# Kernel tuning notes

Hardware: AMD Instinct MI355X
Metric: run time of the kernel (lower is better)

Reference implementation:

```python
import jax, jax.numpy as jnp
import numpy as np

NAF, NBF, DT = 64, 32, 1
B, GROUP = 2000, 100
P = B * GROUP

def _lin(key, din, dout):
    kw, kb = jax.random.split(key)
    return (jax.random.normal(kw, (din, dout), jnp.float32) * 0.02,
            jax.random.normal(kb, (dout,), jnp.float32) * 0.01)

def setup_inputs() -> dict:
    key = jax.random.key(0)
    ks = jax.random.split(key, 12)
    pairs = jax.random.normal(ks[0], (P, 2 * NAF + NBF), jnp.float32)
    idx_pairs = jnp.full((B,), GROUP, dtype=jnp.int32)
    ref_feats = jax.random.normal(ks[1], (B, 32), jnp.float32)
    aw, ab = _lin(ks[2], NAF, 128)
    bw, bb = _lin(ks[3], NBF, 128)
    p1w, p1b = _lin(ks[4], 384, 512)
    p2w, p2b = _lin(ks[5], 512, 256)
    p3w, p3b = _lin(ks[6], 256, 1024)
    f1w, f1b = _lin(ks[7], 1024, 512)
    f2w, f2b = _lin(ks[8], 512, 32)
    f3w, f3b = _lin(ks[9], 32, DT)
    return dict(pairs=pairs, idx_pairs=idx_pairs, ref_feats=ref_feats,
                aw=aw, ab=ab, bw=bw, bb=bb,
                p1w=p1w, p1b=p1b, p2w=p2w, p2b=p2b, p3w=p3w, p3b=p3b,
                f1w=f1w, f1b=f1b, f2w=f2w, f2b=f2b, f3w=f3w, f3b=f3b)

def reference(pairs, idx_pairs, ref_feats,
              aw, ab, bw, bb,
              p1w, p1b, p2w, p2b, p3w, p3b,
              f1w, f1b, f2w, f2b, f3w, f3b):
    relu = jax.nn.relu
    a1 = relu(pairs[:, :NAF] @ aw + ab)            # [P,128]
    a2 = relu(pairs[:, NAF:2 * NAF] @ aw + ab)     # [P,128]
    be = relu(pairs[:, 2 * NAF:] @ bw + bb)        # [P,128]
    h = jnp.concatenate([a1, a2, be], axis=1)      # [P,384]
    h = relu(h @ p1w + p1b)
    h = relu(h @ p2w + p2b)
    x = h @ p3w + p3b                              # [P,1024]
    nb = idx_pairs.shape[0]
    seg = jnp.repeat(jnp.arange(nb, dtype=jnp.int32), idx_pairs,
                     total_repeat_length=x.shape[0])
    sums = jax.ops.segment_sum(x, seg, num_segments=nb)
    h_pair = sums / idx_pairs[:, None].astype(x.dtype)  # segment mean [B,1024]
    h = relu(h_pair @ f1w + f1b)
    h = relu(h @ f2w + f2b)
    return h @ f3w + f3b                           # [B,1]
```

## Files before the change

### kernel.cpp

```cpp
#include <hip/hip_runtime.h>
#include <cstdint>
#include <cstddef>


typedef __bf16 bf16;
typedef __attribute__((ext_vector_type(8))) __bf16 bf16x8;
typedef __attribute__((ext_vector_type(4))) __bf16 bf16x4;
typedef __attribute__((ext_vector_type(4))) float floatx4;
typedef __attribute__((ext_vector_type(16))) float floatx16;

#define GRP 100
#define NWIN 3125

#define WOFF_AW 0
#define WOFF_BW 8192
#define WOFF_P1 12288
#define WOFF_P2 208896
#define WOFF_P3 339968
#define WOFF_F1 602112
#define WOFF_F2 1126400
#define WOFF_HS 1142784

#define LSTR_P  168
#define LSTR_H  392
#define LSTR_H2 136
#define LSTR_MS 264

static __device__ __forceinline__ floatx4 mfma16(bf16x8 a, bf16x8 b, floatx4 c) {
  return __builtin_amdgcn_mfma_f32_16x16x32_bf16(a, b, c, 0, 0, 0);
}
static __device__ __forceinline__ floatx16 mfma32(bf16x8 a, bf16x8 b, floatx16 c) {
  return __builtin_amdgcn_mfma_f32_32x32x16_bf16(a, b, c, 0, 0, 0);
}

static __device__ __forceinline__ void gload(floatx4& d, const bf16* p) {
  asm volatile("global_load_dwordx4 %0, %1, off" : "=v"(d) : "v"(p));
}
static __device__ __forceinline__ bf16x8 bc8(floatx4 v) {
  return __builtin_bit_cast(bf16x8, v);
}

#define VMW(N)                                         \
  do {                                                 \
    asm volatile("s_waitcnt vmcnt(" #N ")");           \
    __builtin_amdgcn_sched_barrier(0);                 \
  } while (0)

#define SYNCL()                                        \
  do {                                                 \
    asm volatile("s_waitcnt lgkmcnt(0)" ::: "memory"); \
    __builtin_amdgcn_s_barrier();                      \
  } while (0)

__global__ __launch_bounds__(256) void pack_lds(
    const float* __restrict__ aw, const float* __restrict__ bw,
    const float* __restrict__ p1w, const float* __restrict__ p2w,
    const float* __restrict__ p3w, const float* __restrict__ f1w,
    const float* __restrict__ f2w, bf16* __restrict__ wpk) {
  __shared__ float t[32][65];
  const int tid = threadIdx.x;
  int b = blockIdx.x;

  if (b < 550) {
    const float* src; int dstoff, K, N, tt;
    bool newf = false;
    if (b < 4)        { src = aw;  dstoff = WOFF_AW; K = 64;   N = 128;  tt = b; }
    else if (b < 6)   { src = bw;  dstoff = WOFF_BW; K = 32;   N = 128;  tt = b - 4; }
    else if (b < 102) { src = p1w; dstoff = WOFF_P1; K = 384;  N = 512;  tt = b - 6;   newf = true; }
    else if (b < 166) { src = p2w; dstoff = WOFF_P2; K = 512;  N = 256;  tt = b - 102; newf = true; }
    else if (b < 294) { src = p3w; dstoff = WOFF_P3; K = 256;  N = 1024; tt = b - 166; }
    else              { src = f1w; dstoff = WOFF_F1; K = 1024; N = 512;  tt = b - 294; }
    const int KT = K >> 5;
    const int kt = tt % KT;
    const int n0 = (tt / KT) * 64;
    for (int i = tid; i < 2048; i += 256) {
      int r = i >> 6, c = i & 63;
      t[r][c] = src[(size_t)(kt * 32 + r) * N + n0 + c];
    }
    __syncthreads();
    if (newf) {
      const int cpp = tid & 63, rb = tid >> 6;
      const int g = (n0 >> 5) + (cpp >> 5);
      const int c = cpp & 31;
      bf16x8 v;
#pragma unroll
      for (int i = 0; i < 8; ++i) v[i] = (bf16)t[rb * 8 + i][cpp];
      *(bf16x8*)(wpk + dstoff +
                 (((size_t)g * KT + kt) * 2 + (rb >> 1)) * 512 +
                 (c + 32 * (rb & 1)) * 8) = v;
    } else {
      const int nc = n0 >> 7, nl0 = n0 & 127;
      bf16* dst = wpk + dstoff + ((size_t)(nc * KT + kt) * 128 + nl0) * 32;
      int o = tid * 8;
      int nl = o >> 5, kk = o & 31;
      bf16x8 v;
#pragma unroll
      for (int i = 0; i < 8; ++i) v[i] = (bf16)t[kk + i][nl];
      *(bf16x8*)(dst + nl * 32 + kk) = v;
    }
  } else {
    const int kt = b - 550;
    for (int i = tid; i < 1024; i += 256) {
      int r = i >> 5, c = i & 31;
      t[r][c] = f2w[(size_t)(kt * 32 + r) * 32 + c];
    }
    __syncthreads();
    if (tid < 128) {
      int o = tid * 8;
      int nl = o >> 5, kk = o & 31;
      bf16x8 v;
#pragma unroll
      for (int i = 0; i < 8; ++i) v[i] = (bf16)t[kk + i][nl];
      *(bf16x8*)(wpk + WOFF_F2 + kt * 1024 + nl * 32 + kk) = v;
    }
  }
}

static __device__ __forceinline__ void kstep2(const bf16* __restrict__ Ab,
                                              int astride, int acol,
                                              const bf16* __restrict__ b0p,
                                              const bf16* __restrict__ b1p,
                                              floatx4* acc, int lm, int lq) {
  bf16x8 b0 = *(const bf16x8*)b0p;
  bf16x8 b1 = *(const bf16x8*)b1p;
#pragma unroll
  for (int mt = 0; mt < 4; ++mt) {
    bf16x8 a = *(const bf16x8*)(Ab + (mt * 16 + lm) * astride + acol + lq * 8);
    acc[mt * 2]     = mfma16(a, b0, acc[mt * 2]);
    acc[mt * 2 + 1] = mfma16(a, b1, acc[mt * 2 + 1]);
  }
}

static __device__ __forceinline__ void epi2(const floatx4* acc,
                                            const float* __restrict__ bias,
                                            bf16* dst, int dstride, int w,
                                            int lm, int lq) {
#pragma unroll
  for (int mt = 0; mt < 4; ++mt)
#pragma unroll
    for (int j = 0; j < 2; ++j) {
      int col = (w + 4 * j) * 16 + lm;
      float bv = bias[col];
      floatx4 c = acc[mt * 2 + j];
#pragma unroll
      for (int r = 0; r < 4; ++r) {
        float v = c[r] + bv;
        v = v > 0.f ? v : 0.f;
        dst[(mt * 16 + lq * 4 + r) * dstride + col] = (bf16)v;
      }
    }
}

__global__ __launch_bounds__(256, 2) void seg_kernel(
    const float* __restrict__ pairs, const float* __restrict__ ab,
    const float* __restrict__ bb, const float* __restrict__ p1b,
    const float* __restrict__ p2b, const bf16* __restrict__ wpk,
    float* __restrict__ hsum) {
  __shared__ __align__(16) bf16 hbuf[64 * LSTR_H];
  __shared__ __align__(16) bf16 pbuf[64 * LSTR_P];

  const int tid = threadIdx.x;
  const int w = tid >> 6;
  const int lane = tid & 63;
  const int lm = lane & 15;
  const int lq = lane >> 4;
  const int l31 = lane & 31;
  const int hi = lane >> 5;
  const int hi8 = hi * 8;
  const int ln8 = lane * 8;
  const int blk = blockIdx.x;

  {
    const float4* src = (const float4*)(pairs + (size_t)blk * (64 * 160));
    for (int i = tid; i < 64 * 40; i += 256) {
      int row = i / 40;
      int c4 = (i - row * 40) * 4;
      float4 v = src[i];
      bf16x4 o = {(bf16)v.x, (bf16)v.y, (bf16)v.z, (bf16)v.w};
      *(bf16x4*)(pbuf + row * LSTR_P + c4) = o;
    }
  }
  SYNCL();

  const floatx4 fz = {0.f, 0.f, 0.f, 0.f};
  const floatx16 fz16 = {0.f, 0.f, 0.f, 0.f, 0.f, 0.f, 0.f, 0.f,
                         0.f, 0.f, 0.f, 0.f, 0.f, 0.f, 0.f, 0.f};
  floatx4 acc[8];

#pragma unroll
  for (int t = 0; t < 8; ++t) acc[t] = fz;
#pragma unroll
  for (int kt = 0; kt < 2; ++kt)
    kstep2(pbuf, LSTR_P, kt * 32,
           wpk + WOFF_AW + ((size_t)(kt * 128 + w * 16 + lm)) * 32 + lq * 8,
           wpk + WOFF_AW + ((size_t)(kt * 128 + (w + 4) * 16 + lm)) * 32 + lq * 8,
           acc, lm, lq);
  epi2(acc, ab, hbuf, LSTR_H, w, lm, lq);
#pragma unroll
  for (int t = 0; t < 8; ++t) acc[t] = fz;
#pragma unroll
  for (int kt = 0; kt < 2; ++kt)
    kstep2(pbuf, LSTR_P, 64 + kt * 32,
           wpk + WOFF_AW + ((size_t)(kt * 128 + w * 16 + lm)) * 32 + lq * 8,
           wpk + WOFF_AW + ((size_t)(kt * 128 + (w + 4) * 16 + lm)) * 32 + lq * 8,
           acc, lm, lq);
  epi2(acc, ab, hbuf + 128, LSTR_H, w, lm, lq);
#pragma unroll
  for (int t = 0; t < 8; ++t) acc[t] = fz;
  kstep2(pbuf, LSTR_P, 128,
         wpk + WOFF_BW + ((size_t)(w * 16 + lm)) * 32 + lq * 8,
         wpk + WOFF_BW + ((size_t)((w + 4) * 16 + lm)) * 32 + lq * 8,
         acc, lm, lq);
  epi2(acc, bb, hbuf + 256, LSTR_H, w, lm, lq);

  float p1bv[4], p2bv[2];
#pragma unroll
  for (int nc = 0; nc < 4; ++nc) p1bv[nc] = p1b[nc * 128 + w * 32 + l31];
  p2bv[0] = p2b[w * 32 + l31];
  p2bv[1] = p2b[(w + 4) * 32 + l31];
  asm volatile("" : "+v"(p1bv[0]), "+v"(p1bv[1]), "+v"(p1bv[2]),
                    "+v"(p1bv[3]), "+v"(p2bv[0]), "+v"(p2bv[1]));

  floatx4 p1r0[4], p1r1[4];
  floatx4 p2r[3][4];
  floatx16 acc3[4];

#pragma unroll
  for (int q = 0; q < 3; ++q) {
    gload(p1r0[q], wpk + WOFF_P1 + (((size_t)w * 12 + q) * 2 + 0) * 512 + ln8);
    gload(p1r1[q], wpk + WOFF_P1 + (((size_t)w * 12 + q) * 2 + 1) * 512 + ln8);
  }
  SYNCL();

#pragma unroll
  for (int t = 0; t < 4; ++t) acc3[t] = fz16;

#pragma unroll
  for (int nc = 0; nc < 4; ++nc) {
    const int gw = nc * 4 + w;
    floatx16 acc2[2];
    acc2[0] = fz16; acc2[1] = fz16;

    {
      bf16x8 an[2][4];
#pragma unroll
      for (int q = 0; q < 2; ++q)
#pragma unroll
        for (int rg = 0; rg < 2; ++rg)
#pragma unroll
          for (int h = 0; h < 2; ++h)
            an[q][rg * 2 + h] = *(const bf16x8*)(
                hbuf + (rg * 32 + l31) * LSTR_H + q * 32 + h * 16 + hi8);
#pragma unroll
      for (int kt = 0; kt < 12; ++kt) {
        bf16x8 a00 = an[kt & 1][0], a01 = an[kt & 1][1];
        bf16x8 a10 = an[kt & 1][2], a11 = an[kt & 1][3];
        if (kt < 10) {
#pragma unroll
          for (int rg = 0; rg < 2; ++rg)
#pragma unroll
            for (int h = 0; h < 2; ++h)
              an[kt & 1][rg * 2 + h] = *(const bf16x8*)(
                  hbuf + (rg * 32 + l31) * LSTR_H + (kt + 2) * 32 + h * 16 + hi8);
        }
        if (kt < 9) {
          gload(p1r0[(kt + 3) & 3],
                wpk + WOFF_P1 + (((size_t)gw * 12 + kt + 3) * 2 + 0) * 512 + ln8);
          gload(p1r1[(kt + 3) & 3],
                wpk + WOFF_P1 + (((size_t)gw * 12 + kt + 3) * 2 + 1) * 512 + ln8);
        }
        if (kt < 9)       { VMW(6); }
        else if (kt == 9) { VMW(4); }
        else if (kt == 10){ VMW(2); }
        else              { VMW(0); }
        __builtin_amdgcn_s_setprio(1);
        bf16x8 b0 = bc8(p1r0[kt & 3]);
        bf16x8 b1 = bc8(p1r1[kt & 3]);
        acc2[0] = mfma32(a00, b0, acc2[0]);
        acc2[1] = mfma32(a10, b0, acc2[1]);
        acc2[0] = mfma32(a01, b1, acc2[0]);
        acc2[1] = mfma32(a11, b1, acc2[1]);
        __builtin_amdgcn_s_setprio(0);
      }
    }

#pragma unroll
    for (int q = 0; q < 2; ++q)
#pragma unroll
      for (int cg = 0; cg < 2; ++cg)
#pragma unroll
        for (int h = 0; h < 2; ++h)
          gload(p2r[q][cg * 2 + h],
                wpk + WOFF_P2 +
                    (((size_t)(cg ? w + 4 : w) * 16 + nc * 4 + q) * 2 + h) * 512 +
                    ln8);

    SYNCL();
    {
      float bv = p1bv[nc];
#pragma unroll
      for (int rg = 0; rg < 2; ++rg)
#pragma unroll
        for (int r = 0; r < 16; ++r) {
          float v = acc2[rg][r] + bv;
          v = v > 0.f ? v : 0.f;
          int row = rg * 32 + (r & 3) + 8 * (r >> 2) + 4 * hi;
          pbuf[row * LSTR_H2 + w * 32 + l31] = (bf16)v;
        }
    }
    SYNCL();

    {
      bf16x8 an2[2][4];
#pragma unroll
      for (int q = 0; q < 2; ++q)
#pragma unroll
        for (int rg = 0; rg < 2; ++rg)
#pragma unroll
          for (int h = 0; h < 2; ++h)
            an2[q][rg * 2 + h] = *(const bf16x8*)(
                pbuf + (rg * 32 + l31) * LSTR_H2 + q * 32 + h * 16 + hi8);
#pragma unroll
      for (int kt2 = 0; kt2 < 4; ++kt2) {
        bf16x8 ac[4];
#pragma unroll
        for (int f = 0; f < 4; ++f) ac[f] = an2[kt2 & 1][f];
        if (kt2 < 2) {
#pragma unroll
          for (int rg = 0; rg < 2; ++rg)
#pragma unroll
            for (int h = 0; h < 2; ++h)
              an2[kt2 & 1][rg * 2 + h] = *(const bf16x8*)(
                  pbuf + (rg * 32 + l31) * LSTR_H2 + (kt2 + 2) * 32 + h * 16 + hi8);
#pragma unroll
          for (int cg = 0; cg < 2; ++cg)
#pragma unroll
            for (int h = 0; h < 2; ++h)
              gload(p2r[(kt2 + 2) % 3][cg * 2 + h],
                    wpk + WOFF_P2 +
                        (((size_t)(cg ? w + 4 : w) * 16 + nc * 4 + kt2 + 2) * 2 + h) *
                            512 + ln8);
        }
        if (kt2 == 1) {
          const int gn = ((nc + 1) & 3) * 4 + w;
#pragma unroll
          for (int q = 0; q < 3; ++q) {
            gload(p1r0[q],
                  wpk + WOFF_P1 + (((size_t)gn * 12 + q) * 2 + 0) * 512 + ln8);
            gload(p1r1[q],
                  wpk + WOFF_P1 + (((size_t)gn * 12 + q) * 2 + 1) * 512 + ln8);
          }
        }
        if (kt2 == 0)      { VMW(8); }
        else if (kt2 == 1) { VMW(14); }
        else if (kt2 == 2) { VMW(10); }
        else               { VMW(6); }
        __builtin_amdgcn_s_setprio(1);
#pragma unroll
        for (int h = 0; h < 2; ++h) {
          bf16x8 b0 = bc8(p2r[kt2 % 3][0 * 2 + h]);
          bf16x8 b1 = bc8(p2r[kt2 % 3][1 * 2 + h]);
          acc3[0] = mfma32(ac[0 * 2 + h], b0, acc3[0]);
          acc3[1] = mfma32(ac[0 * 2 + h], b1, acc3[1]);
          acc3[2] = mfma32(ac[1 * 2 + h], b0, acc3[2]);
          acc3[3] = mfma32(ac[1 * 2 + h], b1, acc3[3]);
        }
        __builtin_amdgcn_s_setprio(0);
      }
    }
  }

  const int s0 = (64 * blk) / 100;
  const int sp = (s0 + 1) * 100 - 64 * blk;

#pragma unroll
  for (int cg = 0; cg < 2; ++cg) {
    float bv = p2bv[cg];
    float tot = 0.f, cs0 = 0.f;
#pragma unroll
    for (int rg = 0; rg < 2; ++rg)
#pragma unroll
      for (int r = 0; r < 16; ++r) {
        float v = acc3[rg * 2 + cg][r] + bv;
        v = v > 0.f ? v : 0.f;
        tot += v;
        int row = rg * 32 + (r & 3) + 8 * (r >> 2) + 4 * hi;
        cs0 += (row < sp) ? v : 0.f;
      }
    float cs1 = tot - cs0;
    cs0 += __shfl_xor(cs0, 32, 64);
    cs1 += __shfl_xor(cs1, 32, 64);
    if (lane < 32) {
      int col = (cg ? w + 4 : w) * 32 + lane;
      hsum[(size_t)(2 * blk) * 256 + col]     = cs0;
      hsum[(size_t)(2 * blk + 1) * 256 + col] = cs1;
    }
  }
}

__global__ __launch_bounds__(512, 2) void tail_kernel(
    const bf16* __restrict__ wpk, const float* __restrict__ hsum,
    const int* __restrict__ idxp, const float* __restrict__ p3b,
    const float* __restrict__ f1b, const float* __restrict__ f2b,
    const float* __restrict__ f3w, const float* __restrict__ f3b,
    float* __restrict__ out) {
  __shared__ __align__(16) bf16 ms[16 * LSTR_MS];
  __shared__ __align__(16) bf16 hp[16 * 1032];
  __shared__ __align__(16) bf16 h2s[16 * 520];
  __shared__ __align__(16) bf16 h3s[16 * 40];

  const int tid = threadIdx.x;
  const int w = tid >> 6;
  const int lane = tid & 63;
  const int lm = lane & 15;
  const int lq = lane >> 4;
  const int r0 = blockIdx.x * 16;
  const floatx4 fz = {0.f, 0.f, 0.f, 0.f};

  for (int i = tid; i < 16 * 64; i += 512) {
    int row = i >> 6, c4 = i & 63;
    int seg = r0 + row;
    int b_lo = (100 * seg) >> 6;
    int b_hi = (100 * seg + 99) >> 6;
    float4 sa = {0.f, 0.f, 0.f, 0.f};
    for (int b = b_lo; b <= b_hi; ++b) {
      int slot = (64 * b >= 100 * seg) ? 0 : 1;
      float4 v = *(const float4*)(hsum + (size_t)(2 * b + slot) * 256 + c4 * 4);
      sa.x += v.x; sa.y += v.y; sa.z += v.z; sa.w += v.w;
    }
    float inv = 1.f / (float)idxp[seg];
    bf16x4 o = {(bf16)(sa.x * inv), (bf16)(sa.y * inv),
                (bf16)(sa.z * inv), (bf16)(sa.w * inv)};
    *(bf16x4*)(ms + row * LSTR_MS + c4 * 4) = o;
  }
  __syncthreads();

#pragma unroll
  for (int nt2 = 0; nt2 < 4; ++nt2) {
    floatx4 a2[2];
    a2[0] = fz; a2[1] = fz;
#pragma unroll
    for (int kt = 0; kt < 8; ++kt) {
      bf16x8 a = *(const bf16x8*)(ms + lm * LSTR_MS + kt * 32 + lq * 8);
#pragma unroll
      for (int j = 0; j < 2; ++j) {
        bf16x8 b = *(const bf16x8*)(wpk + WOFF_P3 +
            ((size_t)((w * 8 + kt) * 128 + (nt2 * 2 + j) * 16 + lm)) * 32 +
            lq * 8);
        a2[j] = mfma16(a, b, a2[j]);
      }
    }
#pragma unroll
    for (int j = 0; j < 2; ++j) {
      int col = w * 128 + (nt2 * 2 + j) * 16 + lm;
      float bv = p3b[col];
#pragma unroll
      for (int r = 0; r < 4; ++r)
        hp[(lq * 4 + r) * 1032 + col] = (bf16)(a2[j][r] + bv);
    }
  }
  __syncthreads();

  {
    floatx4 a4[4];
#pragma unroll
    for (int j = 0; j < 4; ++j) a4[j] = fz;
#pragma unroll 8
    for (int kt = 0; kt < 32; ++kt) {
      bf16x8 a = *(const bf16x8*)(hp + lm * 1032 + kt * 32 + lq * 8);
#pragma unroll
      for (int j = 0; j < 4; ++j) {
        bf16x8 b = *(const bf16x8*)(wpk + WOFF_F1 +
            ((size_t)(((w >> 1) * 32 + kt) * 128 + (w & 1) * 64 + j * 16 + lm)) * 32 +
            lq * 8);
        a4[j] = mfma16(a, b, a4[j]);
      }
    }
#pragma unroll
    for (int j = 0; j < 4; ++j) {
      int col = w * 64 + j * 16 + lm;
      float bv = f1b[col];
#pragma unroll
      for (int r = 0; r < 4; ++r) {
        float v = a4[j][r] + bv;
        v = v > 0.f ? v : 0.f;
        h2s[(lq * 4 + r) * 520 + col] = (bf16)v;
      }
    }
  }
  __syncthreads();

  if (w < 2) {
    floatx4 c2 = fz;
#pragma unroll
    for (int kt = 0; kt < 16; ++kt) {
      bf16x8 a = *(const bf16x8*)(h2s + lm * 520 + kt * 32 + lq * 8);
      bf16x8 b = *(const bf16x8*)(wpk + WOFF_F2 +
                    ((size_t)(kt * 32 + w * 16 + lm)) * 32 + lq * 8);
      c2 = mfma16(a, b, c2);
    }
    int col = w * 16 + lm;
    float bv = f2b[col];
#pragma unroll
    for (int r = 0; r < 4; ++r) {
      float v = c2[r] + bv;
      v = v > 0.f ? v : 0.f;
      h3s[(lq * 4 + r) * 40 + col] = (bf16)v;
    }
  }
  __syncthreads();
  if (w == 0) {
    float ps = 0.f;
#pragma unroll
    for (int jj = 0; jj < 8; ++jj)
      ps += (float)h3s[lm * 40 + lq * 8 + jj] * f3w[lq * 8 + jj];
    ps += __shfl_xor(ps, 16, 64);
    ps += __shfl_xor(ps, 32, 64);
    if (lq == 0) out[r0 + lm] = ps + f3b[0];
  }
}

extern "C" void kernel_launch(void* const* d_in, const int* in_sizes, int n_in,
                              void* d_out, int out_size, void* d_ws,
                              size_t ws_size, hipStream_t stream) {
  (void)in_sizes; (void)n_in; (void)out_size; (void)ws_size;
  const float* pairs = (const float*)d_in[0];
  const int*   idxp  = (const int*)d_in[1];
  const float* aw  = (const float*)d_in[3];
  const float* ab  = (const float*)d_in[4];
  const float* bw  = (const float*)d_in[5];
  const float* bb  = (const float*)d_in[6];
  const float* p1w = (const float*)d_in[7];
  const float* p1b = (const float*)d_in[8];
  const float* p2w = (const float*)d_in[9];
  const float* p2b = (const float*)d_in[10];
  const float* p3w = (const float*)d_in[11];
  const float* p3b = (const float*)d_in[12];
  const float* f1w = (const float*)d_in[13];
  const float* f1b = (const float*)d_in[14];
  const float* f2w = (const float*)d_in[15];
  const float* f2b = (const float*)d_in[16];
  const float* f3w = (const float*)d_in[17];
  const float* f3b = (const float*)d_in[18];

  bf16* wpk = (bf16*)d_ws;
  float* hsum = (float*)(wpk + WOFF_HS);

  pack_lds<<<566, 256, 0, stream>>>(aw, bw, p1w, p2w, p3w, f1w, f2w, wpk);
  seg_kernel<<<NWIN, 256, 0, stream>>>(pairs, ab, bb, p1b, p2b, wpk, hsum);
  tail_kernel<<<125, 512, 0, stream>>>(wpk, hsum, idxp, p3b, f1b, f2b, f3w,
                                       f3b, (float*)d_out);
}
```

Measured before the change: 386.0 us.

## Swizzle LDS layouts, double-buffer p1 output, and move embed layers to 32x32 MFMA

Replaces padded LDS strides with an XOR-swizzled unpadded layout for the input, hidden and intermediate buffers. The intermediate p1 output now alternates between two LDS halves, which removes one block barrier per chunk. The embedding layers are rewritten to use 32x32 MFMA with prepacked weights loaded through the global-load pipeline, so they share the p1 layer's packing format. The aim is fewer bank conflicts, fewer barriers and better latency hiding, at the cost of more complex addressing and higher register use.

Result: slower. 682.2 us (+76.7%).

```diff
diff --git a/kernel.cpp b/kernel.cpp
--- a/kernel.cpp
+++ b/kernel.cpp
@@ -21,10 +21,9 @@
 #define WOFF_F2 1126400
 #define WOFF_HS 1142784
 
-#define LSTR_P  168
-#define LSTR_H  392
-#define LSTR_H2 136
 #define LSTR_MS 264
+
+#define SWZ(row, off) ((off) ^ (((row) & 7) << 4))
 
 static __device__ __forceinline__ floatx4 mfma16(bf16x8 a, bf16x8 b, floatx4 c) {
   return __builtin_amdgcn_mfma_f32_16x16x32_bf16(a, b, c, 0, 0, 0);
@@ -38,6 +37,9 @@
 }
 static __device__ __forceinline__ bf16x8 bc8(floatx4 v) {
   return __builtin_bit_cast(bf16x8, v);
+}
+static __device__ __forceinline__ bf16x8 ldsr(const bf16* b, int byteoff) {
+  return *(const bf16x8*)((const char*)b + byteoff);
 }
 
 #define VMW(N)                                         \
@@ -64,8 +66,8 @@
   if (b < 550) {
     const float* src; int dstoff, K, N, tt;
     bool newf = false;
-    if (b < 4)        { src = aw;  dstoff = WOFF_AW; K = 64;   N = 128;  tt = b; }
-    else if (b < 6)   { src = bw;  dstoff = WOFF_BW; K = 32;   N = 128;  tt = b - 4; }
+    if (b < 4)        { src = aw;  dstoff = WOFF_AW; K = 64;   N = 128;  tt = b;       newf = true; }
+    else if (b < 6)   { src = bw;  dstoff = WOFF_BW; K = 32;   N = 128;  tt = b - 4;   newf = true; }
     else if (b < 102) { src = p1w; dstoff = WOFF_P1; K = 384;  N = 512;  tt = b - 6;   newf = true; }
     else if (b < 166) { src = p2w; dstoff = WOFF_P2; K = 512;  N = 256;  tt = b - 102; newf = true; }
     else if (b < 294) { src = p3w; dstoff = WOFF_P3; K = 256;  N = 1024; tt = b - 166; }
@@ -116,57 +118,20 @@
   }
 }
 
-static __device__ __forceinline__ void kstep2(const bf16* __restrict__ Ab,
-                                              int astride, int acol,
-                                              const bf16* __restrict__ b0p,
-                                              const bf16* __restrict__ b1p,
-                                              floatx4* acc, int lm, int lq) {
-  bf16x8 b0 = *(const bf16x8*)b0p;
-  bf16x8 b1 = *(const bf16x8*)b1p;
-#pragma unroll
-  for (int mt = 0; mt < 4; ++mt) {
-    bf16x8 a = *(const bf16x8*)(Ab + (mt * 16 + lm) * astride + acol + lq * 8);
-    acc[mt * 2]     = mfma16(a, b0, acc[mt * 2]);
-    acc[mt * 2 + 1] = mfma16(a, b1, acc[mt * 2 + 1]);
-  }
-}
-
-static __device__ __forceinline__ void epi2(const floatx4* acc,
-                                            const float* __restrict__ bias,
-                                            bf16* dst, int dstride, int w,
-                                            int lm, int lq) {
-#pragma unroll
-  for (int mt = 0; mt < 4; ++mt)
-#pragma unroll
-    for (int j = 0; j < 2; ++j) {
-      int col = (w + 4 * j) * 16 + lm;
-      float bv = bias[col];
-      floatx4 c = acc[mt * 2 + j];
-#pragma unroll
-      for (int r = 0; r < 4; ++r) {
-        float v = c[r] + bv;
-        v = v > 0.f ? v : 0.f;
-        dst[(mt * 16 + lq * 4 + r) * dstride + col] = (bf16)v;
-      }
-    }
-}
-
 __global__ __launch_bounds__(256, 2) void seg_kernel(
     const float* __restrict__ pairs, const float* __restrict__ ab,
     const float* __restrict__ bb, const float* __restrict__ p1b,
     const float* __restrict__ p2b, const bf16* __restrict__ wpk,
     float* __restrict__ hsum) {
-  __shared__ __align__(16) bf16 hbuf[64 * LSTR_H];
-  __shared__ __align__(16) bf16 pbuf[64 * LSTR_P];
+  __shared__ __align__(16) bf16 hbuf[64 * 384];
+  __shared__ __align__(16) bf16 dbuf[2 * 64 * 128];
 
   const int tid = threadIdx.x;
   const int w = tid >> 6;
   const int lane = tid & 63;
-  const int lm = lane & 15;
-  const int lq = lane >> 4;
   const int l31 = lane & 31;
   const int hi = lane >> 5;
-  const int hi8 = hi * 8;
+  const int hib = hi * 16;
   const int ln8 = lane * 8;
   const int blk = blockIdx.x;
 
@@ -174,62 +139,142 @@
     const float4* src = (const float4*)(pairs + (size_t)blk * (64 * 160));
     for (int i = tid; i < 64 * 40; i += 256) {
       int row = i / 40;
-      int c4 = (i - row * 40) * 4;
+      int c4 = i - row * 40;
       float4 v = src[i];
       bf16x4 o = {(bf16)v.x, (bf16)v.y, (bf16)v.z, (bf16)v.w};
-      *(bf16x4*)(pbuf + row * LSTR_P + c4) = o;
-    }
-  }
-  SYNCL();
-
-  const floatx4 fz = {0.f, 0.f, 0.f, 0.f};
-  const floatx16 fz16 = {0.f, 0.f, 0.f, 0.f, 0.f, 0.f, 0.f, 0.f,
-                         0.f, 0.f, 0.f, 0.f, 0.f, 0.f, 0.f, 0.f};
-  floatx4 acc[8];
-
-#pragma unroll
-  for (int t = 0; t < 8; ++t) acc[t] = fz;
-#pragma unroll
-  for (int kt = 0; kt < 2; ++kt)
-    kstep2(pbuf, LSTR_P, kt * 32,
-           wpk + WOFF_AW + ((size_t)(kt * 128 + w * 16 + lm)) * 32 + lq * 8,
-           wpk + WOFF_AW + ((size_t)(kt * 128 + (w + 4) * 16 + lm)) * 32 + lq * 8,
-           acc, lm, lq);
-  epi2(acc, ab, hbuf, LSTR_H, w, lm, lq);
-#pragma unroll
-  for (int t = 0; t < 8; ++t) acc[t] = fz;
-#pragma unroll
-  for (int kt = 0; kt < 2; ++kt)
-    kstep2(pbuf, LSTR_P, 64 + kt * 32,
-           wpk + WOFF_AW + ((size_t)(kt * 128 + w * 16 + lm)) * 32 + lq * 8,
-           wpk + WOFF_AW + ((size_t)(kt * 128 + (w + 4) * 16 + lm)) * 32 + lq * 8,
-           acc, lm, lq);
-  epi2(acc, ab, hbuf + 128, LSTR_H, w, lm, lq);
-#pragma unroll
-  for (int t = 0; t < 8; ++t) acc[t] = fz;
-  kstep2(pbuf, LSTR_P, 128,
-         wpk + WOFF_BW + ((size_t)(w * 16 + lm)) * 32 + lq * 8,
-         wpk + WOFF_BW + ((size_t)((w + 4) * 16 + lm)) * 32 + lq * 8,
-         acc, lm, lq);
-  epi2(acc, bb, hbuf + 256, LSTR_H, w, lm, lq);
-
+      *(bf16x4*)((char*)dbuf + SWZ(row, row * 384 + c4 * 8)) = o;
+    }
+  }
+
+  float abv = ab[w * 32 + l31];
+  float bbv = bb[w * 32 + l31];
   float p1bv[4], p2bv[2];
 #pragma unroll
   for (int nc = 0; nc < 4; ++nc) p1bv[nc] = p1b[nc * 128 + w * 32 + l31];
   p2bv[0] = p2b[w * 32 + l31];
   p2bv[1] = p2b[(w + 4) * 32 + l31];
-  asm volatile("" : "+v"(p1bv[0]), "+v"(p1bv[1]), "+v"(p1bv[2]),
-                    "+v"(p1bv[3]), "+v"(p2bv[0]), "+v"(p2bv[1]));
-
+  asm volatile("" : "+v"(abv), "+v"(bbv), "+v"(p1bv[0]), "+v"(p1bv[1]),
+                    "+v"(p1bv[2]), "+v"(p1bv[3]), "+v"(p2bv[0]), "+v"(p2bv[1]));
+
+  SYNCL();
+
+  const floatx16 fz16 = {0.f, 0.f, 0.f, 0.f, 0.f, 0.f, 0.f, 0.f,
+                         0.f, 0.f, 0.f, 0.f, 0.f, 0.f, 0.f, 0.f};
   floatx4 p1r0[4], p1r1[4];
   floatx4 p2r[3][4];
+  floatx16 acc2[2];
   floatx16 acc3[4];
 
+  floatx4 eb[6];
+  gload(eb[0], wpk + WOFF_AW + ((size_t)(w * 2 + 0) * 2 + 0) * 512 + ln8);
+  gload(eb[1], wpk + WOFF_AW + ((size_t)(w * 2 + 0) * 2 + 1) * 512 + ln8);
+  gload(eb[2], wpk + WOFF_AW + ((size_t)(w * 2 + 1) * 2 + 0) * 512 + ln8);
+  gload(eb[3], wpk + WOFF_AW + ((size_t)(w * 2 + 1) * 2 + 1) * 512 + ln8);
+  gload(eb[4], wpk + WOFF_BW + ((size_t)(w * 2 + 0)) * 512 + ln8);
+  gload(eb[5], wpk + WOFF_BW + ((size_t)(w * 2 + 1)) * 512 + ln8);
 #pragma unroll
   for (int q = 0; q < 3; ++q) {
     gload(p1r0[q], wpk + WOFF_P1 + (((size_t)w * 12 + q) * 2 + 0) * 512 + ln8);
     gload(p1r1[q], wpk + WOFF_P1 + (((size_t)w * 12 + q) * 2 + 1) * 512 + ln8);
   }
+
+  {
+    bf16x8 af[8];
+#pragma unroll
+    for (int rg = 0; rg < 2; ++rg)
+#pragma unroll
+      for (int kt = 0; kt < 2; ++kt)
+#pragma unroll
+        for (int h = 0; h < 2; ++h) {
+          int row = rg * 32 + l31;
+          af[rg * 4 + kt * 2 + h] =
+              ldsr(dbuf, SWZ(row, row * 384 + kt * 64 + h * 32 + hib));
+        }
+    acc2[0] = fz16; acc2[1] = fz16;
+    VMW(10);
+    __builtin_amdgcn_s_setprio(1);
+#pragma unroll
+    for (int rg = 0; rg < 2; ++rg) {
+      acc2[rg] = mfma32(af[rg * 4 + 0], bc8(eb[0]), acc2[rg]);
+      acc2[rg] = mfma32(af[rg * 4 + 1], bc8(eb[1]), acc2[rg]);
+    }
+    __builtin_amdgcn_s_setprio(0);
+    VMW(8);
+    __builtin_amdgcn_s_setprio(1);
+#pragma unroll
+    for (int rg = 0; rg < 2; ++rg) {
+      acc2[rg] = mfma32(af[rg * 4 + 2], bc8(eb[2]), acc2[rg]);
+      acc2[rg] = mfma32(af[rg * 4 + 3], bc8(eb[3]), acc2[rg]);
+    }
+    __builtin_amdgcn_s_setprio(0);
+#pragma unroll
+    for (int rg = 0; rg < 2; ++rg)
+#pragma unroll
+      for (int r = 0; r < 16; ++r) {
+        float v = acc2[rg][r] + abv;
+        v = v > 0.f ? v : 0.f;
+        int row = rg * 32 + (r & 3) + 8 * (r >> 2) + 4 * hi;
+        *(bf16*)((char*)hbuf + SWZ(row, row * 768 + (w * 32 + l31) * 2)) = (bf16)v;
+      }
+
+#pragma unroll
+    for (int rg = 0; rg < 2; ++rg)
+#pragma unroll
+      for (int kt = 0; kt < 2; ++kt)
+#pragma unroll
+        for (int h = 0; h < 2; ++h) {
+          int row = rg * 32 + l31;
+          af[rg * 4 + kt * 2 + h] =
+              ldsr(dbuf, SWZ(row, row * 384 + 128 + kt * 64 + h * 32 + hib));
+        }
+    acc2[0] = fz16; acc2[1] = fz16;
+    __builtin_amdgcn_s_setprio(1);
+#pragma unroll
+    for (int rg = 0; rg < 2; ++rg) {
+      acc2[rg] = mfma32(af[rg * 4 + 0], bc8(eb[0]), acc2[rg]);
+      acc2[rg] = mfma32(af[rg * 4 + 1], bc8(eb[1]), acc2[rg]);
+      acc2[rg] = mfma32(af[rg * 4 + 2], bc8(eb[2]), acc2[rg]);
+      acc2[rg] = mfma32(af[rg * 4 + 3], bc8(eb[3]), acc2[rg]);
+    }
+    __builtin_amdgcn_s_setprio(0);
+#pragma unroll
+    for (int rg = 0; rg < 2; ++rg)
+#pragma unroll
+      for (int r = 0; r < 16; ++r) {
+        float v = acc2[rg][r] + abv;
+        v = v > 0.f ? v : 0.f;
+        int row = rg * 32 + (r & 3) + 8 * (r >> 2) + 4 * hi;
+        *(bf16*)((char*)hbuf + SWZ(row, row * 768 + (128 + w * 32 + l31) * 2)) = (bf16)v;
+      }
+
+    VMW(6);
+#pragma unroll
+    for (int rg = 0; rg < 2; ++rg)
+#pragma unroll
+      for (int h = 0; h < 2; ++h) {
+        int row = rg * 32 + l31;
+        af[rg * 2 + h] =
+            ldsr(dbuf, SWZ(row, row * 384 + 256 + h * 32 + hib));
+      }
+    acc2[0] = fz16; acc2[1] = fz16;
+    __builtin_amdgcn_s_setprio(1);
+#pragma unroll
+    for (int rg = 0; rg < 2; ++rg) {
+      acc2[rg] = mfma32(af[rg * 2 + 0], bc8(eb[4]), acc2[rg]);
+      acc2[rg] = mfma32(af[rg * 2 + 1], bc8(eb[5]), acc2[rg]);
+    }
+    __builtin_amdgcn_s_setprio(0);
+#pragma unroll
+    for (int rg = 0; rg < 2; ++rg)
+#pragma unroll
+      for (int r = 0; r < 16; ++r) {
+        float v = acc2[rg][r] + bbv;
+        v = v > 0.f ? v : 0.f;
+        int row = rg * 32 + (r & 3) + 8 * (r >> 2) + 4 * hi;
+        *(bf16*)((char*)hbuf + SWZ(row, row * 768 + (256 + w * 32 + l31) * 2)) = (bf16)v;
+      }
+  }
+
   SYNCL();
 
 #pragma unroll
@@ -238,7 +283,6 @@
 #pragma unroll
   for (int nc = 0; nc < 4; ++nc) {
     const int gw = nc * 4 + w;
-    floatx16 acc2[2];
     acc2[0] = fz16; acc2[1] = fz16;
 
     {
@@ -248,9 +292,11 @@
 #pragma unroll
         for (int rg = 0; rg < 2; ++rg)
 #pragma unroll
-          for (int h = 0; h < 2; ++h)
-            an[q][rg * 2 + h] = *(const bf16x8*)(
-                hbuf + (rg * 32 + l31) * LSTR_H + q * 32 + h * 16 + hi8);
+          for (int h = 0; h < 2; ++h) {
+            int row = rg * 32 + l31;
+            an[q][rg * 2 + h] =
+                ldsr(hbuf, SWZ(row, row * 768 + q * 64 + h * 32 + hib));
+          }
 #pragma unroll
       for (int kt = 0; kt < 12; ++kt) {
         bf16x8 a00 = an[kt & 1][0], a01 = an[kt & 1][1];
@@ -259,9 +305,11 @@
 #pragma unroll
           for (int rg = 0; rg < 2; ++rg)
 #pragma unroll
-            for (int h = 0; h < 2; ++h)
-              an[kt & 1][rg * 2 + h] = *(const bf16x8*)(
-                  hbuf + (rg * 32 + l31) * LSTR_H + (kt + 2) * 32 + h * 16 + hi8);
+            for (int h = 0; h < 2; ++h) {
+              int row = rg * 32 + l31;
+              an[kt & 1][rg * 2 + h] = ldsr(
+                  hbuf, SWZ(row, row * 768 + (kt + 2) * 64 + h * 32 + hib));
+            }
         }
         if (kt < 9) {
           gload(p1r0[(kt + 3) & 3],
@@ -295,7 +343,6 @@
                     (((size_t)(cg ? w + 4 : w) * 16 + nc * 4 + q) * 2 + h) * 512 +
                     ln8);
 
-    SYNCL();
     {
       float bv = p1bv[nc];
 #pragma unroll
@@ -305,7 +352,9 @@
           float v = acc2[rg][r] + bv;
           v = v > 0.f ? v : 0.f;
           int row = rg * 32 + (r & 3) + 8 * (r >> 2) + 4 * hi;
-          pbuf[row * LSTR_H2 + w * 32 + l31] = (bf16)v;
+          *(bf16*)((char*)dbuf +
+                   SWZ(row, (nc & 1) * 16384 + row * 256 + (w * 32 + l31) * 2)) =
+              (bf16)v;
         }
     }
     SYNCL();
@@ -317,9 +366,11 @@
 #pragma unroll
         for (int rg = 0; rg < 2; ++rg)
 #pragma unroll
-          for (int h = 0; h < 2; ++h)
-            an2[q][rg * 2 + h] = *(const bf16x8*)(
-                pbuf + (rg * 32 + l31) * LSTR_H2 + q * 32 + h * 16 + hi8);
+          for (int h = 0; h < 2; ++h) {
+            int row = rg * 32 + l31;
+            an2[q][rg * 2 + h] = ldsr(
+                dbuf, SWZ(row, (nc & 1) * 16384 + row * 256 + q * 64 + h * 32 + hib));
+          }
 #pragma unroll
       for (int kt2 = 0; kt2 < 4; ++kt2) {
         bf16x8 ac[4];
@@ -329,9 +380,12 @@
 #pragma unroll
           for (int rg = 0; rg < 2; ++rg)
 #pragma unroll
-            for (int h = 0; h < 2; ++h)
-              an2[kt2 & 1][rg * 2 + h] = *(const bf16x8*)(
-                  pbuf + (rg * 32 + l31) * LSTR_H2 + (kt2 + 2) * 32 + h * 16 + hi8);
+            for (int h = 0; h < 2; ++h) {
+              int row = rg * 32 + l31;
+              an2[kt2 & 1][rg * 2 + h] = ldsr(
+                  dbuf, SWZ(row, (nc & 1) * 16384 + row * 256 + (kt2 + 2) * 64 +
+                                     h * 32 + hib));
+            }
 #pragma unroll
           for (int cg = 0; cg < 2; ++cg)
 #pragma unroll
```

## Use k-chunk-major LDS layout and double-buffer layer-1 output to drop a barrier

Applied to the files above, without the earlier changes.

Changes the LDS activation buffers from padded row-major to a k-chunk-major layout (8-element chunks, 64 rows per chunk), so MFMA operand reads are contiguous 16-byte accesses without padding. The intermediate p1 output buffer is double-buffered by nc parity, which lets one __syncthreads per chunk iteration be removed. The narrow 2-byte scattered epilogue stores may cause more LDS bank conflicts, and the larger shared footprint could affect occupancy.

After: 510.4 us. +32.2%, slower.

```diff
diff --git a/kernel.cpp b/kernel.cpp
--- a/kernel.cpp
+++ b/kernel.cpp
@@ -21,9 +21,6 @@
 #define WOFF_F2 1126400
 #define WOFF_HS 1142784
 
-#define LSTR_P  168
-#define LSTR_H  392
-#define LSTR_H2 136
 #define LSTR_MS 264
 
 static __device__ __forceinline__ floatx4 mfma16(bf16x8 a, bf16x8 b, floatx4 c) {
@@ -116,37 +113,41 @@
   }
 }
 
-static __device__ __forceinline__ void kstep2(const bf16* __restrict__ Ab,
-                                              int astride, int acol,
-                                              const bf16* __restrict__ b0p,
-                                              const bf16* __restrict__ b1p,
-                                              floatx4* acc, int lm, int lq) {
+static __device__ __forceinline__ void ks2f(const bf16* __restrict__ db, int acol,
+                                            const bf16* __restrict__ b0p,
+                                            const bf16* __restrict__ b1p,
+                                            floatx4* acc, int lm, int lq) {
   bf16x8 b0 = *(const bf16x8*)b0p;
   bf16x8 b1 = *(const bf16x8*)b1p;
+  const int ko = (acol >> 3) + lq;
 #pragma unroll
   for (int mt = 0; mt < 4; ++mt) {
-    bf16x8 a = *(const bf16x8*)(Ab + (mt * 16 + lm) * astride + acol + lq * 8);
+    int row = mt * 16 + lm;
+    bf16x8 a = *(const bf16x8*)(db + (ko * 64 + row) * 8);
     acc[mt * 2]     = mfma16(a, b0, acc[mt * 2]);
     acc[mt * 2 + 1] = mfma16(a, b1, acc[mt * 2 + 1]);
   }
 }
 
-static __device__ __forceinline__ void epi2(const floatx4* acc,
-                                            const float* __restrict__ bias,
-                                            bf16* dst, int dstride, int w,
-                                            int lm, int lq) {
+static __device__ __forceinline__ void epi2f(const floatx4* acc,
+                                             const float* __restrict__ bias,
+                                             bf16* __restrict__ hb, int colbase,
+                                             int w, int lm, int lq) {
 #pragma unroll
   for (int mt = 0; mt < 4; ++mt)
 #pragma unroll
     for (int j = 0; j < 2; ++j) {
-      int col = (w + 4 * j) * 16 + lm;
-      float bv = bias[col];
-      floatx4 c = acc[mt * 2 + j];
+      int c = (w + 4 * j) * 16 + lm;
+      float bv = bias[c];
+      floatx4 cc = acc[mt * 2 + j];
+      int k = colbase + c;
+      int base = (k >> 3) * 512 + (k & 7);
 #pragma unroll
       for (int r = 0; r < 4; ++r) {
-        float v = c[r] + bv;
+        float v = cc[r] + bv;
         v = v > 0.f ? v : 0.f;
-        dst[(mt * 16 + lq * 4 + r) * dstride + col] = (bf16)v;
+        int row = mt * 16 + lq * 4 + r;
+        hb[base + row * 8] = (bf16)v;
       }
     }
 }
@@ -156,8 +157,8 @@
     const float* __restrict__ bb, const float* __restrict__ p1b,
     const float* __restrict__ p2b, const bf16* __restrict__ wpk,
     float* __restrict__ hsum) {
-  __shared__ __align__(16) bf16 hbuf[64 * LSTR_H];
-  __shared__ __align__(16) bf16 pbuf[64 * LSTR_P];
+  __shared__ __align__(16) bf16 hbuf[64 * 384];
+  __shared__ __align__(16) bf16 dbuf[2 * 64 * 128];
 
   const int tid = threadIdx.x;
   const int w = tid >> 6;
@@ -166,7 +167,6 @@
   const int lq = lane >> 4;
   const int l31 = lane & 31;
   const int hi = lane >> 5;
-  const int hi8 = hi * 8;
   const int ln8 = lane * 8;
   const int blk = blockIdx.x;
 
@@ -174,10 +174,10 @@
     const float4* src = (const float4*)(pairs + (size_t)blk * (64 * 160));
     for (int i = tid; i < 64 * 40; i += 256) {
       int row = i / 40;
-      int c4 = (i - row * 40) * 4;
+      int c4 = i - row * 40;
       float4 v = src[i];
       bf16x4 o = {(bf16)v.x, (bf16)v.y, (bf16)v.z, (bf16)v.w};
-      *(bf16x4*)(pbuf + row * LSTR_P + c4) = o;
+      *(bf16x4*)(dbuf + ((c4 >> 1) * 64 + row) * 8 + (c4 & 1) * 4) = o;
     }
   }
   SYNCL();
@@ -191,27 +191,27 @@
   for (int t = 0; t < 8; ++t) acc[t] = fz;
 #pragma unroll
   for (int kt = 0; kt < 2; ++kt)
-    kstep2(pbuf, LSTR_P, kt * 32,
-           wpk + WOFF_AW + ((size_t)(kt * 128 + w * 16 + lm)) * 32 + lq * 8,
-           wpk + WOFF_AW + ((size_t)(kt * 128 + (w + 4) * 16 + lm)) * 32 + lq * 8,
-           acc, lm, lq);
-  epi2(acc, ab, hbuf, LSTR_H, w, lm, lq);
+    ks2f(dbuf, kt * 32,
+         wpk + WOFF_AW + ((size_t)(kt * 128 + w * 16 + lm)) * 32 + lq * 8,
+         wpk + WOFF_AW + ((size_t)(kt * 128 + (w + 4) * 16 + lm)) * 32 + lq * 8,
+         acc, lm, lq);
+  epi2f(acc, ab, hbuf, 0, w, lm, lq);
 #pragma unroll
   for (int t = 0; t < 8; ++t) acc[t] = fz;
 #pragma unroll
   for (int kt = 0; kt < 2; ++kt)
-    kstep2(pbuf, LSTR_P, 64 + kt * 32,
-           wpk + WOFF_AW + ((size_t)(kt * 128 + w * 16 + lm)) * 32 + lq * 8,
-           wpk + WOFF_AW + ((size_t)(kt * 128 + (w + 4) * 16 + lm)) * 32 + lq * 8,
-           acc, lm, lq);
-  epi2(acc, ab, hbuf + 128, LSTR_H, w, lm, lq);
+    ks2f(dbuf, 64 + kt * 32,
+         wpk + WOFF_AW + ((size_t)(kt * 128 + w * 16 + lm)) * 32 + lq * 8,
+         wpk + WOFF_AW + ((size_t)(kt * 128 + (w + 4) * 16 + lm)) * 32 + lq * 8,
+         acc, lm, lq);
+  epi2f(acc, ab, hbuf, 128, w, lm, lq);
 #pragma unroll
   for (int t = 0; t < 8; ++t) acc[t] = fz;
-  kstep2(pbuf, LSTR_P, 128,
-         wpk + WOFF_BW + ((size_t)(w * 16 + lm)) * 32 + lq * 8,
-         wpk + WOFF_BW + ((size_t)((w + 4) * 16 + lm)) * 32 + lq * 8,
-         acc, lm, lq);
-  epi2(acc, bb, hbuf + 256, LSTR_H, w, lm, lq);
+  ks2f(dbuf, 128,
+       wpk + WOFF_BW + ((size_t)(w * 16 + lm)) * 32 + lq * 8,
+       wpk + WOFF_BW + ((size_t)((w + 4) * 16 + lm)) * 32 + lq * 8,
+       acc, lm, lq);
+  epi2f(acc, bb, hbuf, 256, w, lm, lq);
 
   float p1bv[4], p2bv[2];
 #pragma unroll
@@ -223,6 +223,7 @@
 
   floatx4 p1r0[4], p1r1[4];
   floatx4 p2r[3][4];
+  floatx16 acc2[2];
   floatx16 acc3[4];
 
 #pragma unroll
@@ -235,10 +236,12 @@
 #pragma unroll
   for (int t = 0; t < 4; ++t) acc3[t] = fz16;
 
+  const int ckb = ((w * 32 + l31) >> 3) * 512 + ((w * 32 + l31) & 7);
+
 #pragma unroll
   for (int nc = 0; nc < 4; ++nc) {
     const int gw = nc * 4 + w;
-    floatx16 acc2[2];
+    bf16* ch = dbuf + (nc & 1) * 8192;
     acc2[0] = fz16; acc2[1] = fz16;
 
     {
@@ -250,7 +253,7 @@
 #pragma unroll
           for (int h = 0; h < 2; ++h)
             an[q][rg * 2 + h] = *(const bf16x8*)(
-                hbuf + (rg * 32 + l31) * LSTR_H + q * 32 + h * 16 + hi8);
+                hbuf + ((q * 4 + h * 2 + hi) * 64 + rg * 32 + l31) * 8);
 #pragma unroll
       for (int kt = 0; kt < 12; ++kt) {
         bf16x8 a00 = an[kt & 1][0], a01 = an[kt & 1][1];
@@ -261,7 +264,7 @@
 #pragma unroll
             for (int h = 0; h < 2; ++h)
               an[kt & 1][rg * 2 + h] = *(const bf16x8*)(
-                  hbuf + (rg * 32 + l31) * LSTR_H + (kt + 2) * 32 + h * 16 + hi8);
+                  hbuf + (((kt + 2) * 4 + h * 2 + hi) * 64 + rg * 32 + l31) * 8);
         }
         if (kt < 9) {
           gload(p1r0[(kt + 3) & 3],
@@ -295,7 +298,6 @@
                     (((size_t)(cg ? w + 4 : w) * 16 + nc * 4 + q) * 2 + h) * 512 +
                     ln8);
 
-    SYNCL();
     {
       float bv = p1bv[nc];
 #pragma unroll
@@ -305,7 +307,7 @@
           float v = acc2[rg][r] + bv;
           v = v > 0.f ? v : 0.f;
           int row = rg * 32 + (r & 3) + 8 * (r >> 2) + 4 * hi;
-          pbuf[row * LSTR_H2 + w * 32 + l31] = (bf16)v;
+          ch[ckb + row * 8] = (bf16)v;
         }
     }
     SYNCL();
@@ -319,7 +321,7 @@
 #pragma unroll
           for (int h = 0; h < 2; ++h)
             an2[q][rg * 2 + h] = *(const bf16x8*)(
-                pbuf + (rg * 32 + l31) * LSTR_H2 + q * 32 + h * 16 + hi8);
+                ch + ((q * 4 + h * 2 + hi) * 64 + rg * 32 + l31) * 8);
 #pragma unroll
       for (int kt2 = 0; kt2 < 4; ++kt2) {
         bf16x8 ac[4];
@@ -331,7 +333,7 @@
 #pragma unroll
             for (int h = 0; h < 2; ++h)
               an2[kt2 & 1][rg * 2 + h] = *(const bf16x8*)(
-                  pbuf + (rg * 32 + l31) * LSTR_H2 + (kt2 + 2) * 32 + h * 16 + hi8);
+                  ch + (((kt2 + 2) * 4 + h * 2 + hi) * 64 + rg * 32 + l31) * 8);
 #pragma unroll
           for (int cg = 0; cg < 2; ++cg)
 #pragma unroll
```
